# Optimization experiments

Measured on AMD Instinct MI355X. Metric: run time of the kernel, lower is better.

The kernel has to match this reference:

```python
import jax, jax.numpy as jnp
import numpy as np
from math import sqrt

LOCAL_WINDOW = 32
STRIDE = 64


def _sparse_mask(L):
    # L_Q == L_K path of DozerAttention:
    #  - local window: diagonals at offsets 0..local_window//2 (both signs)
    #  - strided: diagonals at offsets 0, stride+1, 2*(stride+1), ... (both signs)
    i = jnp.arange(L)[:, None]
    j = jnp.arange(L)[None, :]
    d = jnp.abs(i - j)
    local = d <= (LOCAL_WINDOW // 2)
    strided = (d % (STRIDE + 1)) == 0
    return (local | strided).astype(jnp.float32)  # [L, L]


def setup_inputs() -> dict:
    key = jax.random.key(0)
    B, L, H, D = 2, 2048, 8, 64
    kq, kk, kv = jax.random.split(key, 3)
    queries = jax.random.normal(kq, (B, L, H, D), dtype=jnp.float32)
    keys = jax.random.normal(kk, (B, L, H, D), dtype=jnp.float32)
    values = jax.random.normal(kv, (B, L, H, D), dtype=jnp.float32)
    # TriangularCausalMask: True above the diagonal -> masked with -inf
    causal = jnp.triu(jnp.ones((L, L), dtype=bool), k=1)
    attn_mask = jnp.broadcast_to(causal[None, None], (B, 1, L, L))
    return {"queries": queries, "keys": keys, "values": values, "attn_mask": attn_mask}


def reference(queries, keys, values, attn_mask):
    B, L, H, D = queries.shape
    scale = 1.0 / sqrt(D)
    sm = _sparse_mask(L)  # [L, L]
    # Original fills a zero-initialized dense score tensor only at selected key
    # columns per query row; equivalent to dense QK^T elementwise-masked by sm
    # (non-selected entries stay exactly 0, NOT -inf -- faithful quirk).
    scores = jnp.einsum('blhe,bshe->bhls', queries, keys) * sm  # [B,H,L,L]
    scores = jnp.where(attn_mask, -jnp.inf, scores)
    A = jax.nn.softmax(scale * scores, axis=-1)  # dropout p=0.0 in this config
    V = jnp.einsum('bhls,bshd->blhd', A, values)  # [B,L,H,D]
    return V
```

## Files before the change

### kernel.cpp

```cpp
#include <hip/hip_runtime.h>
#include <hip/hip_bf16.h>

#define B_ 2
#define L_ 2048
#define H_ 8
#define D_ 64
#define SP_ 65
#define NC_ 128
#define NL2_ 8
#define RS_ 512

typedef __attribute__((ext_vector_type(8))) short bf16x8;
typedef __attribute__((ext_vector_type(16))) float f32x16;

static __device__ inline short f2bf(float x) {
    return __builtin_bit_cast(short, __float2bfloat16(x));
}

static __device__ inline bf16x8 ld8_bf16(const float* __restrict__ p) {
    float4 a = *(const float4*)p;
    float4 b = *(const float4*)(p + 4);
    bf16x8 r;
    r[0]=f2bf(a.x); r[1]=f2bf(a.y); r[2]=f2bf(a.z); r[3]=f2bf(a.w);
    r[4]=f2bf(b.x); r[5]=f2bf(b.y); r[6]=f2bf(b.z); r[7]=f2bf(b.w);
    return r;
}

__global__ void chunk_sums_k(const float* __restrict__ v, float* __restrict__ csum1) {
    int blk = blockIdx.x;
    int c  = blk % NC_;
    int bh = blk / NC_;
    int h = bh % H_, b = bh / H_;
    int d = threadIdx.x;
    float s = 0.f;
    int l0 = c * 16;
    #pragma unroll
    for (int l = 0; l < 16; ++l)
        s += v[((size_t)(b * L_ + l0 + l) * H_ + h) * D_ + d];
    csum1[(bh * NC_ + c) * D_ + d] = s;
}

__global__ void l2_sums_k(const float* __restrict__ csum1, float* __restrict__ csum2) {
    int blk = blockIdx.x;
    int c2 = blk % NL2_;
    int bh = blk / NL2_;
    int d  = threadIdx.x;
    float s = 0.f;
    #pragma unroll
    for (int cc = 0; cc < 16; ++cc)
        s += csum1[(bh * NC_ + c2 * 16 + cc) * D_ + d];
    csum2[(bh * NL2_ + c2) * D_ + d] = s;
}

__global__ __launch_bounds__(64) void local_k(const float* __restrict__ q,
                                              const float* __restrict__ kk,
                                              const float* __restrict__ v,
                                              const float* __restrict__ csum1,
                                              const float* __restrict__ csum2,
                                              float* __restrict__ pA,
                                              float* __restrict__ zA) {
    __shared__ float Pw[32][68];

    int lane = threadIdx.x;
    int half = lane >> 5, ln = lane & 31;
    int bh = blockIdx.x >> 6;
    int T  = (blockIdx.x & 63) << 5;
    int h = bh & 7, b = bh >> 3;

    const size_t base = (size_t)b * L_ * RS_ + (size_t)h * D_;

    const float* qrow = q + base + (size_t)(T + ln) * RS_;
    bf16x8 aq[4];
    #pragma unroll
    for (int kb = 0; kb < 4; ++kb) aq[kb] = ld8_bf16(qrow + kb * 16 + half * 8);

    int j0 = T - 16 + ln; j0 = j0 < 0 ? 0 : j0;
    int j1 = T + 16 + ln; j1 = j1 > L_ - 1 ? L_ - 1 : j1;
    const float* kr0 = kk + base + (size_t)j0 * RS_;
    const float* kr1 = kk + base + (size_t)j1 * RS_;
    f32x16 acc0 = {}; f32x16 acc1 = {};
    #pragma unroll
    for (int kb = 0; kb < 4; ++kb) {
        bf16x8 b0 = ld8_bf16(kr0 + kb * 16 + half * 8);
        bf16x8 b1 = ld8_bf16(kr1 + kb * 16 + half * 8);
        acc0 = __builtin_amdgcn_mfma_f32_32x32x16_bf16(aq[kb], b0, acc0, 0, 0, 0);
        acc1 = __builtin_amdgcn_mfma_f32_32x32x16_bf16(aq[kb], b1, acc1, 0, 0, 0);
    }

    #pragma unroll
    for (int r = 0; r < 16; ++r) {
        int m = (r & 3) + 8 * (r >> 2) + 4 * half;
        bool a0 = (ln >= m) && (ln <= m + 16) && (T - 16 + ln >= 0);
        float w0 = a0 ? (__expf(0.125f * acc0[r]) - 1.f) : 0.f;
        if ((m < 16) && (ln >= 16) && (ln <= m + 16)) w0 += 1.f;
        bool a1 = (ln <= m - 16);
        float w1 = a1 ? (__expf(0.125f * acc1[r]) - 1.f) : 0.f;
        if ((m >= 16) && (ln <= m - 16)) w1 += 1.f;
        Pw[m][ln]      = w0;
        Pw[m][32 + ln] = w1;
    }
    __syncthreads();

    f32x16 p0 = {}; f32x16 p1 = {}; f32x16 po = {};
    bf16x8 ones = {};
    if (ln == 0) { short o = f2bf(1.f); for (int t = 0; t < 8; ++t) ones[t] = o; }
    #pragma unroll
    for (int kb = 0; kb < 4; ++kb) {
        int k0 = kb * 16 + half * 8;
        const float* pr = &Pw[ln][k0];
        float4 x = *(const float4*)pr;
        float4 y = *(const float4*)(pr + 4);
        bf16x8 ap;
        ap[0]=f2bf(x.x); ap[1]=f2bf(x.y); ap[2]=f2bf(x.z); ap[3]=f2bf(x.w);
        ap[4]=f2bf(y.x); ap[5]=f2bf(y.y); ap[6]=f2bf(y.z); ap[7]=f2bf(y.w);
        bf16x8 bv0, bv1;
        #pragma unroll
        for (int jj = 0; jj < 8; ++jj) {
            int c = k0 + jj;
            int jr = T - 16 + c;
            jr = jr < 0 ? 0 : (jr > L_ - 1 ? L_ - 1 : jr);
            const float* vr = v + base + (size_t)jr * RS_;
            bv0[jj] = f2bf(vr[ln]);
            bv1[jj] = f2bf(vr[32 + ln]);
        }
        p0 = __builtin_amdgcn_mfma_f32_32x32x16_bf16(ap, bv0, p0, 0, 0, 0);
        p1 = __builtin_amdgcn_mfma_f32_32x32x16_bf16(ap, bv1, p1, 0, 0, 0);
        po = __builtin_amdgcn_mfma_f32_32x32x16_bf16(ap, ones, po, 0, 0, 0);
    }

    int c2n = T >> 8;
    int c1a = (T >> 8) << 4, c1b = T >> 4;
    const float* cs2 = csum2 + (size_t)bh * NL2_ * D_;
    const float* cs1 = csum1 + (size_t)bh * NC_ * D_;
    float pr0 = 0.f, pr1 = 0.f;
    for (int cc = 0; cc < c2n; ++cc) {
        pr0 += cs2[cc * D_ + ln]; pr1 += cs2[cc * D_ + 32 + ln];
    }
    for (int cc = c1a; cc < c1b; ++cc) {
        pr0 += cs1[cc * D_ + ln]; pr1 += cs1[cc * D_ + 32 + ln];
    }
    float ch0 = cs1[c1b * D_ + ln], ch1 = cs1[c1b * D_ + 32 + ln];

    float* pArow = pA + (size_t)bh * L_ * D_;
    float* zrow  = zA + (size_t)bh * L_;
    #pragma unroll
    for (int r = 0; r < 16; ++r) {
        int m = (r & 3) + 8 * (r >> 2) + 4 * half;
        int i = T + m;
        float e0 = pr0 + ((m & 16) ? ch0 : 0.f);
        float e1 = pr1 + ((m & 16) ? ch1 : 0.f);
        pArow[(size_t)i * D_ + ln]      = p0[r] + e0;
        pArow[(size_t)i * D_ + 32 + ln] = p1[r] + e1;
        if (ln == 0) zrow[i] = po[r] - (float)((m & 15) + 1);
    }
}

__global__ __launch_bounds__(64) void strided_k(const float* __restrict__ q,
                                                const float* __restrict__ kk,
                                                const float* __restrict__ v,
                                                const float* __restrict__ pA,
                                                const float* __restrict__ zA,
                                                float* __restrict__ out) {
    __shared__ float Pw[32][36];

    int lane = threadIdx.x;
    int half = lane >> 5, ln = lane & 31;
    int bh = blockIdx.x / SP_;
    int r  = blockIdx.x % SP_;
    int h = bh & 7, b = bh >> 3;

    const size_t base = (size_t)b * L_ * RS_ + (size_t)h * D_;

    int lq = r + SP_ * ln;
    int lqc = lq > L_ - 1 ? L_ - 1 : lq;
    const float* qrow = q  + base + (size_t)lqc * RS_;
    const float* krow = kk + base + (size_t)lqc * RS_;

    f32x16 acc = {};
    #pragma unroll
    for (int kb = 0; kb < 4; ++kb) {
        bf16x8 a  = ld8_bf16(qrow + kb * 16 + half * 8);
        bf16x8 bb = ld8_bf16(krow + kb * 16 + half * 8);
        acc = __builtin_amdgcn_mfma_f32_32x32x16_bf16(a, bb, acc, 0, 0, 0);
    }

    #pragma unroll
    for (int rg = 0; rg < 16; ++rg) {
        int m = (rg & 3) + 8 * (rg >> 2) + 4 * half;
        bool act = (ln < m) && (r + SP_ * m < L_);
        float w = act ? (__expf(0.125f * acc[rg]) - 1.f) : 0.f;
        Pw[m][ln] = w;
    }
    __syncthreads();

    f32x16 p0 = {}; f32x16 p1 = {}; f32x16 po = {};
    bf16x8 ones = {};
    if (ln == 0) { short o = f2bf(1.f); for (int t = 0; t < 8; ++t) ones[t] = o; }
    #pragma unroll
    for (int kb = 0; kb < 2; ++kb) {
        int k0 = kb * 16 + half * 8;
        const float* pr = &Pw[ln][k0];
        float4 x = *(const float4*)pr;
        float4 y = *(const float4*)(pr + 4);
        bf16x8 ap;
        ap[0]=f2bf(x.x); ap[1]=f2bf(x.y); ap[2]=f2bf(x.z); ap[3]=f2bf(x.w);
        ap[4]=f2bf(y.x); ap[5]=f2bf(y.y); ap[6]=f2bf(y.z); ap[7]=f2bf(y.w);
        bf16x8 bv0, bv1;
        #pragma unroll
        for (int jj = 0; jj < 8; ++jj) {
            int s = k0 + jj;
            int lv = r + SP_ * s;
            lv = lv > L_ - 1 ? L_ - 1 : lv;
            const float* vr = v + base + (size_t)lv * RS_;
            bv0[jj] = f2bf(vr[ln]);
            bv1[jj] = f2bf(vr[32 + ln]);
        }
        p0 = __builtin_amdgcn_mfma_f32_32x32x16_bf16(ap, bv0, p0, 0, 0, 0);
        p1 = __builtin_amdgcn_mfma_f32_32x32x16_bf16(ap, bv1, p1, 0, 0, 0);
        po = __builtin_amdgcn_mfma_f32_32x32x16_bf16(ap, ones, po, 0, 0, 0);
    }

    const float* pArow = pA + (size_t)bh * L_ * D_;
    const float* zrow  = zA + (size_t)bh * L_;
    #pragma unroll
    for (int rg = 0; rg < 16; ++rg) {
        int m = (rg & 3) + 8 * (rg >> 2) + 4 * half;
        int l = r + SP_ * m;
        if (l < L_) {
            float zb = __shfl(po[rg], lane & 32, 64);
            float inv = 1.f / (zrow[l] + zb + (float)(l + 1));
            float o0 = (p0[rg] + pArow[(size_t)l * D_ + ln]) * inv;
            float o1 = (p1[rg] + pArow[(size_t)l * D_ + 32 + ln]) * inv;
            out[base + (size_t)l * RS_ + ln]      = o0;
            out[base + (size_t)l * RS_ + 32 + ln] = o1;
        }
    }
}

extern "C" void kernel_launch(void* const* d_in, const int* in_sizes, int n_in,
                              void* d_out, int out_size, void* d_ws, size_t ws_size,
                              hipStream_t stream) {
    const float* q = (const float*)d_in[0];
    const float* k = (const float*)d_in[1];
    const float* v = (const float*)d_in[2];
    float* out = (float*)d_out;

    float* csum1 = (float*)d_ws;
    float* csum2 = csum1 + (size_t)B_ * H_ * NC_ * D_;
    float* pA    = csum2 + (size_t)B_ * H_ * NL2_ * D_;
    float* zA    = pA    + (size_t)B_ * H_ * L_ * D_;

    chunk_sums_k<<<B_ * H_ * NC_, 64, 0, stream>>>(v, csum1);
    l2_sums_k   <<<B_ * H_ * NL2_, 64, 0, stream>>>(csum1, csum2);

    local_k  <<<B_ * H_ * (L_ / 32), 64, 0, stream>>>(q, k, v, csum1, csum2, pA, zA);
    strided_k<<<B_ * H_ * SP_,       64, 0, stream>>>(q, k, v, pA, zA, out);
}
```

Before: 118.1 us.

## Fuse chunk sums with strided pass and finalize output in local kernel

Folds the two V chunk-sum kernels and the strided-attention pass into one launch with role-dispatched blocks, so the level-2 sums are now computed straight from V instead of from level-1 sums. The local kernel becomes the final stage that combines the strided partials and writes the normalized output. Four-wave blocks replace single-wave blocks, and V fragments are loaded into registers before the QK MFMA so the loads can overlap compute. This cuts the number of launches from four to two and removes the scattered strided-row epilogue, at the cost of more register pressure and some redundant V reads for the level-2 sums.

```diff
diff --git a/kernel.cpp b/kernel.cpp
--- a/kernel.cpp
+++ b/kernel.cpp
@@ -26,48 +26,150 @@
     return r;
 }
 
-__global__ void chunk_sums_k(const float* __restrict__ v, float* __restrict__ csum1) {
-    int blk = blockIdx.x;
-    int c  = blk % NC_;
-    int bh = blk / NC_;
-    int h = bh % H_, b = bh / H_;
-    int d = threadIdx.x;
-    float s = 0.f;
-    int l0 = c * 16;
-    #pragma unroll
-    for (int l = 0; l < 16; ++l)
-        s += v[((size_t)(b * L_ + l0 + l) * H_ + h) * D_ + d];
-    csum1[(bh * NC_ + c) * D_ + d] = s;
-}
-
-__global__ void l2_sums_k(const float* __restrict__ csum1, float* __restrict__ csum2) {
-    int blk = blockIdx.x;
-    int c2 = blk % NL2_;
-    int bh = blk / NL2_;
-    int d  = threadIdx.x;
-    float s = 0.f;
-    #pragma unroll
-    for (int cc = 0; cc < 16; ++cc)
-        s += csum1[(bh * NC_ + c2 * 16 + cc) * D_ + d];
-    csum2[(bh * NL2_ + c2) * D_ + d] = s;
-}
-
-__global__ __launch_bounds__(64) void local_k(const float* __restrict__ q,
-                                              const float* __restrict__ kk,
-                                              const float* __restrict__ v,
-                                              const float* __restrict__ csum1,
-                                              const float* __restrict__ csum2,
-                                              float* __restrict__ pA,
-                                              float* __restrict__ zA) {
-    __shared__ float Pw[32][68];
-
-    int lane = threadIdx.x;
+static __device__ inline bf16x8 ones_frag() {
+    bf16x8 r;
+    short o = f2bf(1.f);
+    #pragma unroll
+    for (int t = 0; t < 8; ++t) r[t] = o;
+    return r;
+}
+
+__global__ __launch_bounds__(256) void pre_strided_k(const float* __restrict__ q,
+                                                     const float* __restrict__ kk,
+                                                     const float* __restrict__ v,
+                                                     float* __restrict__ csum1,
+                                                     float* __restrict__ csum2,
+                                                     float* __restrict__ pB,
+                                                     float* __restrict__ zB) {
+    __shared__ float Pw[4][32][36];
+    int wib  = threadIdx.x >> 6;
+    int lane = threadIdx.x & 63;
+    int blk  = blockIdx.x;
+
+    if (blk < 260) {
+        int u  = blk * 4 + wib;
+        int bh = u / SP_;
+        int r  = u % SP_;
+        int h = bh & 7, b = bh >> 3;
+        int half = lane >> 5, ln = lane & 31;
+        const size_t base = (size_t)b * L_ * RS_ + (size_t)h * D_;
+
+        bf16x8 bv0[2], bv1[2];
+        #pragma unroll
+        for (int kb = 0; kb < 2; ++kb) {
+            int k0 = kb * 16 + half * 8;
+            #pragma unroll
+            for (int jj = 0; jj < 8; ++jj) {
+                int lv = r + SP_ * (k0 + jj);
+                lv = lv > L_ - 1 ? L_ - 1 : lv;
+                const float* vr = v + base + (size_t)lv * RS_;
+                bv0[kb][jj] = f2bf(vr[ln]);
+                bv1[kb][jj] = f2bf(vr[32 + ln]);
+            }
+        }
+
+        int lq = r + SP_ * ln;
+        int lqc = lq > L_ - 1 ? L_ - 1 : lq;
+        const float* qrow = q  + base + (size_t)lqc * RS_;
+        const float* krow = kk + base + (size_t)lqc * RS_;
+        f32x16 acc = {};
+        #pragma unroll
+        for (int kb = 0; kb < 4; ++kb) {
+            bf16x8 a  = ld8_bf16(qrow + kb * 16 + half * 8);
+            bf16x8 bb = ld8_bf16(krow + kb * 16 + half * 8);
+            acc = __builtin_amdgcn_mfma_f32_32x32x16_bf16(a, bb, acc, 0, 0, 0);
+        }
+        #pragma unroll
+        for (int rg = 0; rg < 16; ++rg) {
+            int m = (rg & 3) + 8 * (rg >> 2) + 4 * half;
+            bool act = (ln < m) && (r + SP_ * m < L_);
+            Pw[wib][m][ln] = act ? (__expf(0.125f * acc[rg]) - 1.f) : 0.f;
+        }
+        __syncthreads();
+
+        f32x16 p0 = {}; f32x16 p1 = {}; f32x16 po = {};
+        bf16x8 ones = ones_frag();
+        #pragma unroll
+        for (int kb = 0; kb < 2; ++kb) {
+            int k0 = kb * 16 + half * 8;
+            const float* pr = &Pw[wib][ln][k0];
+            float4 x = *(const float4*)pr;
+            float4 y = *(const float4*)(pr + 4);
+            bf16x8 ap;
+            ap[0]=f2bf(x.x); ap[1]=f2bf(x.y); ap[2]=f2bf(x.z); ap[3]=f2bf(x.w);
+            ap[4]=f2bf(y.x); ap[5]=f2bf(y.y); ap[6]=f2bf(y.z); ap[7]=f2bf(y.w);
+            p0 = __builtin_amdgcn_mfma_f32_32x32x16_bf16(ap, bv0[kb], p0, 0, 0, 0);
+            p1 = __builtin_amdgcn_mfma_f32_32x32x16_bf16(ap, bv1[kb], p1, 0, 0, 0);
+            po = __builtin_amdgcn_mfma_f32_32x32x16_bf16(ap, ones,    po, 0, 0, 0);
+        }
+        float* pBr = pB + (size_t)bh * L_ * D_;
+        float* zBr = zB + (size_t)bh * L_;
+        #pragma unroll
+        for (int rg = 0; rg < 16; ++rg) {
+            int m = (rg & 3) + 8 * (rg >> 2) + 4 * half;
+            int l = r + SP_ * m;
+            if (l < L_) {
+                pBr[(size_t)l * D_ + ln]      = p0[rg];
+                pBr[(size_t)l * D_ + 32 + ln] = p1[rg];
+                if (ln == 0) zBr[l] = po[rg];
+            }
+        }
+    } else if (blk < 772) {
+        int u = (blk - 260) * 4 + wib;
+        int c = u & (NC_ - 1);
+        int bh = u >> 7;
+        int h = bh & 7, b = bh >> 3;
+        const float* vb = v + (size_t)(b * L_ + c * 16) * RS_ + h * D_ + lane;
+        float s = 0.f;
+        #pragma unroll
+        for (int l = 0; l < 16; ++l) s += vb[l * RS_];
+        csum1[(size_t)u * D_ + lane] = s;
+    } else {
+        int u = (blk - 772) * 4 + wib;
+        int c2 = u & 7;
+        int bh = u >> 3;
+        int h = bh & 7, b = bh >> 3;
+        const float* vb = v + (size_t)(b * L_ + c2 * 256) * RS_ + h * D_ + lane;
+        float s0 = 0.f, s1 = 0.f, s2 = 0.f, s3 = 0.f;
+        for (int l = 0; l < 256; l += 4) {
+            s0 += vb[(l + 0) * RS_]; s1 += vb[(l + 1) * RS_];
+            s2 += vb[(l + 2) * RS_]; s3 += vb[(l + 3) * RS_];
+        }
+        csum2[(size_t)u * D_ + lane] = (s0 + s1) + (s2 + s3);
+    }
+}
+
+__global__ __launch_bounds__(256) void local_final_k(const float* __restrict__ q,
+                                                     const float* __restrict__ kk,
+                                                     const float* __restrict__ v,
+                                                     const float* __restrict__ csum1,
+                                                     const float* __restrict__ csum2,
+                                                     const float* __restrict__ pB,
+                                                     const float* __restrict__ zB,
+                                                     float* __restrict__ out) {
+    __shared__ float Pw[4][32][68];
+    int wib  = threadIdx.x >> 6;
+    int lane = threadIdx.x & 63;
     int half = lane >> 5, ln = lane & 31;
-    int bh = blockIdx.x >> 6;
-    int T  = (blockIdx.x & 63) << 5;
+    int tile = blockIdx.x * 4 + wib;
+    int bh = tile >> 6;
+    int T  = (tile & 63) << 5;
     int h = bh & 7, b = bh >> 3;
-
     const size_t base = (size_t)b * L_ * RS_ + (size_t)h * D_;
+
+    bf16x8 bv0[4], bv1[4];
+    #pragma unroll
+    for (int kb = 0; kb < 4; ++kb) {
+        int k0 = kb * 16 + half * 8;
+        #pragma unroll
+        for (int jj = 0; jj < 8; ++jj) {
+            int jr = T - 16 + k0 + jj;
+            jr = jr < 0 ? 0 : (jr > L_ - 1 ? L_ - 1 : jr);
+            const float* vr = v + base + (size_t)jr * RS_;
+            bv0[kb][jj] = f2bf(vr[ln]);
+            bv1[kb][jj] = f2bf(vr[32 + ln]);
+        }
+    }
 
     const float* qrow = q + base + (size_t)(T + ln) * RS_;
     bf16x8 aq[4];
@@ -96,36 +198,25 @@
         bool a1 = (ln <= m - 16);
         float w1 = a1 ? (__expf(0.125f * acc1[r]) - 1.f) : 0.f;
         if ((m >= 16) && (ln <= m - 16)) w1 += 1.f;
-        Pw[m][ln]      = w0;
-        Pw[m][32 + ln] = w1;
+        Pw[wib][m][ln]      = w0;
+        Pw[wib][m][32 + ln] = w1;
     }
     __syncthreads();
 
     f32x16 p0 = {}; f32x16 p1 = {}; f32x16 po = {};
-    bf16x8 ones = {};
-    if (ln == 0) { short o = f2bf(1.f); for (int t = 0; t < 8; ++t) ones[t] = o; }
+    bf16x8 ones = ones_frag();
     #pragma unroll
     for (int kb = 0; kb < 4; ++kb) {
         int k0 = kb * 16 + half * 8;
-        const float* pr = &Pw[ln][k0];
+        const float* pr = &Pw[wib][ln][k0];
         float4 x = *(const float4*)pr;
         float4 y = *(const float4*)(pr + 4);
         bf16x8 ap;
         ap[0]=f2bf(x.x); ap[1]=f2bf(x.y); ap[2]=f2bf(x.z); ap[3]=f2bf(x.w);
         ap[4]=f2bf(y.x); ap[5]=f2bf(y.y); ap[6]=f2bf(y.z); ap[7]=f2bf(y.w);
-        bf16x8 bv0, bv1;
-        #pragma unroll
-        for (int jj = 0; jj < 8; ++jj) {
-            int c = k0 + jj;
-            int jr = T - 16 + c;
-            jr = jr < 0 ? 0 : (jr > L_ - 1 ? L_ - 1 : jr);
-            const float* vr = v + base + (size_t)jr * RS_;
-            bv0[jj] = f2bf(vr[ln]);
-            bv1[jj] = f2bf(vr[32 + ln]);
-        }
-        p0 = __builtin_amdgcn_mfma_f32_32x32x16_bf16(ap, bv0, p0, 0, 0, 0);
-        p1 = __builtin_amdgcn_mfma_f32_32x32x16_bf16(ap, bv1, p1, 0, 0, 0);
-        po = __builtin_amdgcn_mfma_f32_32x32x16_bf16(ap, ones, po, 0, 0, 0);
+        p0 = __builtin_amdgcn_mfma_f32_32x32x16_bf16(ap, bv0[kb], p0, 0, 0, 0);
+        p1 = __builtin_amdgcn_mfma_f32_32x32x16_bf16(ap, bv1[kb], p1, 0, 0, 0);
+        po = __builtin_amdgcn_mfma_f32_32x32x16_bf16(ap, ones,    po, 0, 0, 0);
     }
 
     int c2n = T >> 8;
@@ -141,99 +232,18 @@
     }
     float ch0 = cs1[c1b * D_ + ln], ch1 = cs1[c1b * D_ + 32 + ln];
 
-    float* pArow = pA + (size_t)bh * L_ * D_;
-    float* zrow  = zA + (size_t)bh * L_;
+    const float* pBr = pB + (size_t)bh * L_ * D_;
+    const float* zBr = zB + (size_t)bh * L_;
     #pragma unroll
     for (int r = 0; r < 16; ++r) {
         int m = (r & 3) + 8 * (r >> 2) + 4 * half;
         int i = T + m;
         float e0 = pr0 + ((m & 16) ? ch0 : 0.f);
         float e1 = pr1 + ((m & 16) ? ch1 : 0.f);
-        pArow[(size_t)i * D_ + ln]      = p0[r] + e0;
-        pArow[(size_t)i * D_ + 32 + ln] = p1[r] + e1;
-        if (ln == 0) zrow[i] = po[r] - (float)((m & 15) + 1);
-    }
-}
-
-__global__ __launch_bounds__(64) void strided_k(const float* __restrict__ q,
-                                                const float* __restrict__ kk,
-                                                const float* __restrict__ v,
-                                                const float* __restrict__ pA,
-                                                const float* __restrict__ zA,
-                                                float* __restrict__ out) {
-    __shared__ float Pw[32][36];
-
-    int lane = threadIdx.x;
-    int half = lane >> 5, ln = lane & 31;
-    int bh = blockIdx.x / SP_;
-    int r  = blockIdx.x % SP_;
-    int h = bh & 7, b = bh >> 3;
-
-    const size_t base = (size_t)b * L_ * RS_ + (size_t)h * D_;
-
-    int lq = r + SP_ * ln;
-    int lqc = lq > L_ - 1 ? L_ - 1 : lq;
-    const float* qrow = q  + base + (size_t)lqc * RS_;
-    const float* krow = kk + base + (size_t)lqc * RS_;
-
-    f32x16 acc = {};
-    #pragma unroll
-    for (int kb = 0; kb < 4; ++kb) {
-        bf16x8 a  = ld8_bf16(qrow + kb * 16 + half * 8);
-        bf16x8 bb = ld8_bf16(krow + kb * 16 + half * 8);
-        acc = __builtin_amdgcn_mfma_f32_32x32x16_bf16(a, bb, acc, 0, 0, 0);
-    }
-
-    #pragma unroll
-    for (int rg = 0; rg < 16; ++rg) {
-        int m = (rg & 3) + 8 * (rg >> 2) + 4 * half;
-        bool act = (ln < m) && (r + SP_ * m < L_);
-        float w = act ? (__expf(0.125f * acc[rg]) - 1.f) : 0.f;
-        Pw[m][ln] = w;
-    }
-    __syncthreads();
-
-    f32x16 p0 = {}; f32x16 p1 = {}; f32x16 po = {};
-    bf16x8 ones = {};
-    if (ln == 0) { short o = f2bf(1.f); for (int t = 0; t < 8; ++t) ones[t] = o; }
-    #pragma unroll
-    for (int kb = 0; kb < 2; ++kb) {
-        int k0 = kb * 16 + half * 8;
-        const float* pr = &Pw[ln][k0];
-        float4 x = *(const float4*)pr;
-        float4 y = *(const float4*)(pr + 4);
-        bf16x8 ap;
-        ap[0]=f2bf(x.x); ap[1]=f2bf(x.y); ap[2]=f2bf(x.z); ap[3]=f2bf(x.w);
-        ap[4]=f2bf(y.x); ap[5]=f2bf(y.y); ap[6]=f2bf(y.z); ap[7]=f2bf(y.w);
-        bf16x8 bv0, bv1;
-        #pragma unroll
-        for (int jj = 0; jj < 8; ++jj) {
-            int s = k0 + jj;
-            int lv = r + SP_ * s;
-            lv = lv > L_ - 1 ? L_ - 1 : lv;
-            const float* vr = v + base + (size_t)lv * RS_;
-            bv0[jj] = f2bf(vr[ln]);
-            bv1[jj] = f2bf(vr[32 + ln]);
-        }
-        p0 = __builtin_amdgcn_mfma_f32_32x32x16_bf16(ap, bv0, p0, 0, 0, 0);
-        p1 = __builtin_amdgcn_mfma_f32_32x32x16_bf16(ap, bv1, p1, 0, 0, 0);
-        po = __builtin_amdgcn_mfma_f32_32x32x16_bf16(ap, ones, po, 0, 0, 0);
-    }
-
-    const float* pArow = pA + (size_t)bh * L_ * D_;
-    const float* zrow  = zA + (size_t)bh * L_;
-    #pragma unroll
-    for (int rg = 0; rg < 16; ++rg) {
-        int m = (rg & 3) + 8 * (rg >> 2) + 4 * half;
-        int l = r + SP_ * m;
-        if (l < L_) {
-            float zb = __shfl(po[rg], lane & 32, 64);
-            float inv = 1.f / (zrow[l] + zb + (float)(l + 1));
-            float o0 = (p0[rg] + pArow[(size_t)l * D_ + ln]) * inv;
-            float o1 = (p1[rg] + pArow[(size_t)l * D_ + 32 + ln]) * inv;
-            out[base + (size_t)l * RS_ + ln]      = o0;
-            out[base + (size_t)l * RS_ + 32 + ln] = o1;
-        }
+        float zloc = po[r] - (float)((m & 15) + 1);
+        float inv = 1.f / (zloc + zBr[i] + (float)(i + 1));
+        out[base + (size_t)i * RS_ + ln]      = (p0[r] + e0 + pBr[(size_t)i * D_ + ln])      * inv;
+        out[base + (size_t)i * RS_ + 32 + ln] = (p1[r] + e1 + pBr[(size_t)i * D_ + 32 + ln]) * inv;
     }
 }
 
@@ -247,12 +257,9 @@
 
     float* csum1 = (float*)d_ws;
     float* csum2 = csum1 + (size_t)B_ * H_ * NC_ * D_;
-    float* pA    = csum2 + (size_t)B_ * H_ * NL2_ * D_;
-    float* zA    = pA    + (size_t)B_ * H_ * L_ * D_;
-
-    chunk_sums_k<<<B_ * H_ * NC_, 64, 0, stream>>>(v, csum1);
-    l2_sums_k   <<<B_ * H_ * NL2_, 64, 0, stream>>>(csum1, csum2);
-
-    local_k  <<<B_ * H_ * (L_ / 32), 64, 0, stream>>>(q, k, v, csum1, csum2, pA, zA);
-    strided_k<<<B_ * H_ * SP_,       64, 0, stream>>>(q, k, v, pA, zA, out);
-}
+    float* pB    = csum2 + (size_t)B_ * H_ * NL2_ * D_;
+    float* zB    = pB    + (size_t)B_ * H_ * L_ * D_;
+
+    pre_strided_k<<<804, 256, 0, stream>>>(q, k, v, csum1, csum2, pB, zB);
+    local_final_k<<<256, 256, 0, stream>>>(q, k, v, csum1, csum2, pB, zB, out);
+}
```

Result: no change. 115.8 us (-2.0%).
